# Performance work log

Measured on AMD Instinct MI355X. Metric: run time of the kernel, lower is better.

Reference implementation:

```python
import jax, jax.numpy as jnp
import numpy as np
import math

B, S, HID, H = 8, 512, 768, 12
D = HID // H  # 64
LABEL_VOCAB = 2 * 40 + 1  # 81
EPS = 1e-5


def layernorm(x, g, b):
    mu = jnp.mean(x, axis=-1, keepdims=True)
    var = jnp.var(x, axis=-1, keepdims=True)
    return (x - mu) * jax.lax.rsqrt(var + EPS) * g + b


def setup_inputs() -> dict:
    key = jax.random.key(0)
    ks = jax.random.split(key, 12)
    s = 0.02
    return {
        "hidden_states": jax.random.normal(ks[0], (B, S, HID), jnp.float32),
        "attention_mask": jnp.zeros((B, 1, 1, S), jnp.float32),
        "graph_arc": jax.random.randint(ks[1], (B, S, S), 0, LABEL_VOCAB, jnp.int32),
        "Wq": jax.random.normal(ks[2], (HID, HID), jnp.float32) * s,
        "bq": jnp.zeros((HID,), jnp.float32),
        "Wk": jax.random.normal(ks[3], (HID, HID), jnp.float32) * s,
        "bk": jnp.zeros((HID,), jnp.float32),
        "Wv": jax.random.normal(ks[4], (HID, HID), jnp.float32) * s,
        "bv": jnp.zeros((HID,), jnp.float32),
        "rel_k": jax.random.normal(ks[5], (LABEL_VOCAB, D), jnp.float32) * s,
        "rel_v": jax.random.normal(ks[6], (LABEL_VOCAB, D), jnp.float32) * s,
        "ln_k_g": jnp.ones((D,), jnp.float32),
        "ln_k_b": jnp.zeros((D,), jnp.float32),
        "ln_v_g": jnp.ones((D,), jnp.float32),
        "ln_v_b": jnp.zeros((D,), jnp.float32),
    }


def reference(hidden_states, attention_mask, graph_arc, Wq, bq, Wk, bk, Wv, bv,
              rel_k, rel_v, ln_k_g, ln_k_b, ln_v_g, ln_v_b):
    # projections -> [B, H, S, D]
    def split_heads(x):
        return x.reshape(B, S, H, D).transpose(0, 2, 1, 3)

    q = split_heads(hidden_states @ Wq + bq)
    k = split_heads(hidden_states @ Wk + bk)
    v = split_heads(hidden_states @ Wv + bv)

    # relation embeddings [B, S, S, D], layernormed over D
    dp_keys = layernorm(rel_k[graph_arc], ln_k_g, ln_k_b)
    dp_values = layernorm(rel_v[graph_arc], ln_v_g, ln_v_b)

    scores = jnp.einsum('bhqd,bhkd->bhqk', q, k) / math.sqrt(D)
    # relative_matmul_dp: per (b, q-position) GEMM of q[B,S,H,D] with dp_keys^T
    scores = scores + jnp.einsum('bqhd,bqkd->bhqk', q.transpose(0, 2, 1, 3), dp_keys)
    scores = scores + attention_mask

    probs = jax.nn.softmax(scores, axis=-1)  # dropout p=0 (eval)

    ctx = jnp.einsum('bhqk,bhkd->bqhd', probs, v)
    # relative_matmul_dpv
    ctx = ctx + jnp.einsum('bhqk,bqkd->bqhd', probs, dp_values)
    return ctx.reshape(B, S, HID)
```

## Files before the change

### kernel.cpp

```cpp
#include <hip/hip_runtime.h>
#include <hip/hip_bf16.h>

#define BB 8
#define SS 512
#define HIDV 768
#define HH 12
#define DD 64
#define LV 81

typedef __attribute__((ext_vector_type(8))) short short8v;
typedef __attribute__((ext_vector_type(4))) short short4v;
typedef __attribute__((ext_vector_type(4))) float f32x4;

#define MFMA16(a, b, c) __builtin_amdgcn_mfma_f32_16x16x32_bf16(a, b, c, 0, 0, 0)

__device__ __forceinline__ short f2bf(float f) {
    __hip_bfloat16 h = __float2bfloat16(f);
    return *reinterpret_cast<short*>(&h);
}
__device__ __forceinline__ float bf2f(short s) {
    __hip_bfloat16 h = *reinterpret_cast<__hip_bfloat16*>(&s);
    return __bfloat162float(h);
}
__device__ __forceinline__ void gload16(const void* g, void* l) {
    __builtin_amdgcn_global_load_lds((const __attribute__((address_space(1))) void*)g,
                                     (__attribute__((address_space(3))) void*)l, 16, 0, 0);
}

__global__ __launch_bounds__(256) void prep_ln_kernel(
    const float* __restrict__ rel_k, const float* __restrict__ rel_v,
    const float* __restrict__ gk, const float* __restrict__ bk,
    const float* __restrict__ gv, const float* __restrict__ bv,
    short* __restrict__ lnkb, short* __restrict__ lnvT) {
    __shared__ float ln_lds[2 * LV][DD];
    int t = threadIdx.x;
    if (t < 2 * LV) {
        bool isv = (t >= LV);
        int r = isv ? t - LV : t;
        const float* row = (isv ? rel_v : rel_k) + r * DD;
        const float* g = isv ? gv : gk;
        const float* be = isv ? bv : bk;
        float mu = 0.f;
        for (int d = 0; d < DD; ++d) mu += row[d];
        mu *= (1.f / DD);
        float var = 0.f;
        for (int d = 0; d < DD; ++d) { float x = row[d] - mu; var += x * x; }
        var *= (1.f / DD);
        float rs = rsqrtf(var + 1e-5f);
        for (int d = 0; d < DD; ++d) ln_lds[t][d] = (row[d] - mu) * rs * g[d] + be[d];
    }
    __syncthreads();
    for (int i = t; i < 96 * DD; i += 256) {
        int l = i >> 6, d = i & 63;
        lnkb[i] = (l < LV) ? f2bf(ln_lds[l][d]) : (short)0;
    }
    for (int i = t; i < DD * 96; i += 256) {
        int d = i / 96, ll = i - d * 96;
        lnvT[i] = (ll < LV) ? f2bf(ln_lds[LV + ll][d]) : (short)0;
    }
}

__global__ __launch_bounds__(256) void conv_hidden_kernel(const float* __restrict__ in,
                                                          short* __restrict__ out) {
    int i = (blockIdx.x * 256 + threadIdx.x) * 4;
    float4 v = *reinterpret_cast<const float4*>(&in[i]);
    short4v o; o[0] = f2bf(v.x); o[1] = f2bf(v.y); o[2] = f2bf(v.z); o[3] = f2bf(v.w);
    *reinterpret_cast<short4v*>(&out[i]) = o;
}

__global__ __launch_bounds__(256) void transw_kernel(
    const float* __restrict__ Wq, const float* __restrict__ Wk, const float* __restrict__ Wv,
    short* __restrict__ WqT, short* __restrict__ WkT, short* __restrict__ WvT) {
    const float* W; short* O;
    if (blockIdx.z == 0) { W = Wq; O = WqT; }
    else if (blockIdx.z == 1) { W = Wk; O = WkT; }
    else { W = Wv; O = WvT; }
    __shared__ float tile[32][33];
    int k0 = blockIdx.y * 32, n0 = blockIdx.x * 32;
    int t = threadIdx.x;
    int r = t >> 3, c4 = (t & 7) * 4;
    float4 v = *reinterpret_cast<const float4*>(&W[(size_t)(k0 + r) * HIDV + n0 + c4]);
    tile[r][c4 + 0] = v.x; tile[r][c4 + 1] = v.y; tile[r][c4 + 2] = v.z; tile[r][c4 + 3] = v.w;
    __syncthreads();
    short4v o;
    o[0] = f2bf(tile[c4 + 0][r]); o[1] = f2bf(tile[c4 + 1][r]);
    o[2] = f2bf(tile[c4 + 2][r]); o[3] = f2bf(tile[c4 + 3][r]);
    *reinterpret_cast<short4v*>(&O[(size_t)(n0 + r) * HIDV + k0 + c4]) = o;
}

__global__ __launch_bounds__(256) void qkv_gemm_kernel(
    const short* __restrict__ Abf,
    const short* __restrict__ WqT, const short* __restrict__ WkT, const short* __restrict__ WvT,
    const float* __restrict__ bq, const float* __restrict__ bk, const float* __restrict__ bv,
    short* __restrict__ qo, short* __restrict__ ko, short* __restrict__ vto) {
    const short* Bt; const float* bias;
    int z = blockIdx.z;
    if (z == 0) { Bt = WqT; bias = bq; }
    else if (z == 1) { Bt = WkT; bias = bk; }
    else { Bt = WvT; bias = bv; }

    __shared__ short smem[8192];
    short* As = smem;
    short* Bs = smem + 4096;

    const int tid = threadIdx.x;
    const int lane = tid & 63, w = tid >> 6;
    const int li = lane & 15, g = lane >> 4;
    const int wr = w >> 1, wc = w & 1;
    const int m0 = blockIdx.y * 64, n0 = blockIdx.x * 64;

    f32x4 acc[2][2];
    for (int ra = 0; ra < 2; ++ra)
        for (int cb = 0; cb < 2; ++cb)
            for (int r = 0; r < 4; ++r) acc[ra][cb][r] = 0.f;

#pragma unroll 1
    for (int k0 = 0; k0 < HIDV; k0 += 64) {
#pragma unroll
        for (int j = 0; j < 2; ++j) {
            int c = j * 256 + tid;
            int row = c >> 3, s = c & 7;
            int src = s ^ (row & 7);
// ... 38 lines not shown
                float bv_ = bias[n0 + n];
#pragma unroll
                for (int r = 0; r < 4; ++r) {
                    int m = m0 + 32 * wr + 16 * ra + 4 * g + r;
                    int s = m & 511;
                    dst[(((size_t)bidx * HH + h) * SS + s) * DD + n] =
                        f2bf((acc[ra][cb][r] + bv_) * sc);
                }
            }
    } else {
        short* Cs = smem;
#pragma unroll
        for (int ra = 0; ra < 2; ++ra)
#pragma unroll
            for (int cb = 0; cb < 2; ++cb) {
                int nl = 32 * wc + 16 * cb + li;
                float bv_ = bias[n0 + nl];
#pragma unroll
                for (int r = 0; r < 4; ++r) {
                    int ml = 32 * wr + 16 * ra + 4 * g + r;
                    Cs[nl * 72 + ml] = f2bf(acc[ra][cb][r] + bv_);
                }
            }
        __syncthreads();
        for (int c = tid; c < 512; c += 256) {
            int dl = c >> 3, s8 = (c & 7) * 8;
            short8v vv = *reinterpret_cast<const short8v*>(&Cs[dl * 72 + s8]);
            *reinterpret_cast<short8v*>(
                &vto[(((size_t)bidx * HH + h) * DD + dl) * SS + (m0 & 511) + s8]) = vv;
        }
    }
}

__global__ __launch_bounds__(256, 2) void attn_kernel(
    const short* __restrict__ qb, const short* __restrict__ kb, const short* __restrict__ vt,
    const int* __restrict__ arc, const float* __restrict__ mask,
    const short* __restrict__ lnkb, const short* __restrict__ lnvT,
    float* __restrict__ outp) {
    __shared__ short Ks[2][64][64];
    __shared__ short Vs[64][64];
    __shared__ float qlds[4][16][82];
    __shared__ float bucket[4][16][96];
    __shared__ short pl[4][16][72];

    const int tid = threadIdx.x;
    const int w = tid >> 6, lane = tid & 63;
    const int li = lane & 15, g = lane >> 4;
    const int bx = blockIdx.x;
    const int b = bx & 7;
    const int rest = bx >> 3;
    const int h = rest % HH, qt = rest / HH;
    const int bh = b * HH + h;
    const int q0 = qt * 64 + w * 16;

    const short* kbp = kb + (size_t)bh * SS * DD;
    const short* vbp = vt + (size_t)bh * DD * SS;
    const int* arcb = arc + ((size_t)b * SS + qt * 64) * SS;
    const float* maskb = mask + b * SS;

#pragma unroll
    for (int j = 0; j < 2; ++j) {
        int c = tid + 256 * j, row = c >> 3, s8 = (c & 7) ^ (row & 7);
        gload16(kbp + (size_t)row * DD + s8 * 8, &Ks[0][0][0] + c * 8);
    }
    for (int i = lane; i < 16 * 96; i += 64) (&bucket[w][0][0])[i] = 0.f;

    short8v qf[2];
    {
        const short* qrow = qb + ((size_t)bh * SS + q0 + li) * DD + 8 * g;
        qf[0] = *reinterpret_cast<const short8v*>(qrow);
        qf[1] = *reinterpret_cast<const short8v*>(qrow + 32);
    }

    {
        f32x4 qr[6];
        __builtin_amdgcn_s_setprio(1);
#pragma unroll
        for (int ct = 0; ct < 6; ++ct) {
            f32x4 a = {0.f, 0.f, 0.f, 0.f};
            short8v b0 = *reinterpret_cast<const short8v*>(&lnkb[(16 * ct + li) * DD + 8 * g]);
            short8v b1 = *reinterpret_cast<const short8v*>(&lnkb[(16 * ct + li) * DD + 32 + 8 * g]);
            a = MFMA16(qf[0], b0, a);
            a = MFMA16(qf[1], b1, a);
            qr[ct] = a;
        }
        __builtin_amdgcn_s_setprio(0);
#pragma unroll
        for (int ct = 0; ct < 6; ++ct)
#pragma unroll
            for (int r = 0; r < 4; ++r)
                if (16 * ct + li < 82) qlds[w][4 * g + r][16 * ct + li] = qr[ct][r];
    }

    f32x4 oacc[4];
    for (int t = 0; t < 4; ++t) for (int r = 0; r < 4; ++r) oacc[t][r] = 0.f;
    float lsum[4] = {0.f, 0.f, 0.f, 0.f};

#pragma unroll
    for (int kt = 0; kt < 8; ++kt) {
        const int cur = kt & 1, nxt = cur ^ 1;
        const int kb0 = kt * 64;

#pragma unroll
        for (int j = 0; j < 2; ++j) {
            int c = tid + 256 * j, row = c >> 3, s8 = (c & 7) ^ (row & 7);
            gload16(vbp + (size_t)row * SS + kb0 + s8 * 8, &Vs[0][0] + c * 8);
        }
        if (kt < 7) {
#pragma unroll
            for (int j = 0; j < 2; ++j) {
                int c = tid + 256 * j, row = c >> 3, s8 = (c & 7) ^ (row & 7);
                gload16(kbp + (size_t)(kb0 + 64 + row) * DD + s8 * 8, &Ks[nxt][0][0] + c * 8);
            }
            asm volatile("s_waitcnt vmcnt(4)" ::: "memory");
        } else {
            asm volatile("s_waitcnt vmcnt(2)" ::: "memory");
        }
        __builtin_amdgcn_sched_barrier(0);
        __builtin_amdgcn_s_barrier();
        __builtin_amdgcn_sched_barrier(0);

        int arcv[16];
        float mv[4];
#pragma unroll
        for (int t = 0; t < 4; ++t) {
            mv[t] = maskb[kb0 + 16 * t + li];
#pragma unroll
            for (int r = 0; r < 4; ++r)
                arcv[4 * t + r] = arcb[(size_t)(w * 16 + 4 * g + r) * SS + kb0 + 16 * t + li];
        }

        f32x4 sacc[4];
        __builtin_amdgcn_s_setprio(1);
#pragma unroll
        for (int t = 0; t < 4; ++t) {
            int row = 16 * t + li;
            short8v kf0 = *reinterpret_cast<const short8v*>(&Ks[cur][row][((g) ^ (li & 7)) * 8]);
            short8v kf1 = *reinterpret_cast<const short8v*>(&Ks[cur][row][((4 + g) ^ (li & 7)) * 8]);
            f32x4 a = {0.f, 0.f, 0.f, 0.f};
            a = MFMA16(qf[0], kf0, a);
            a = MFMA16(qf[1], kf1, a);
            sacc[t] = a;
        }
        __builtin_amdgcn_s_setprio(0);

#pragma unroll
        for (int t = 0; t < 4; ++t) {
#pragma unroll
            for (int r = 0; r < 4; ++r) {
                const int a_ = arcv[4 * t + r];
                const int row = 4 * g + r;
                float s = sacc[t][r] + qlds[w][row][a_] + mv[t];
                float p = __expf(s);
                lsum[r] += p;
                atomicAdd(&bucket[w][row][a_], p);
                pl[w][row][16 * t + li] = f2bf(p);
            }
        }

        if (kt < 7) asm volatile("s_waitcnt vmcnt(2)" ::: "memory");
        else        asm volatile("s_waitcnt vmcnt(0)" ::: "memory");
        __builtin_amdgcn_sched_barrier(0);
        __builtin_amdgcn_s_barrier();
        __builtin_amdgcn_sched_barrier(0);

        short8v pf0 = *reinterpret_cast<const short8v*>(&pl[w][li][8 * g]);
        short8v pf1 = *reinterpret_cast<const short8v*>(&pl[w][li][8 * g + 32]);
        __builtin_amdgcn_s_setprio(1);
#pragma unroll
        for (int t2 = 0; t2 < 4; ++t2) {
            int row = 16 * t2 + li;
            short8v vf0 = *reinterpret_cast<const short8v*>(&Vs[row][((g) ^ (li & 7)) * 8]);
            short8v vf1 = *reinterpret_cast<const short8v*>(&Vs[row][((4 + g) ^ (li & 7)) * 8]);
            oacc[t2] = MFMA16(pf0, vf0, oacc[t2]);
            oacc[t2] = MFMA16(pf1, vf1, oacc[t2]);
        }
        __builtin_amdgcn_s_setprio(0);

        if (kt < 7) {
            __builtin_amdgcn_s_barrier();
            __builtin_amdgcn_sched_barrier(0);
        }
    }

#pragma unroll
    for (int off = 1; off < 16; off <<= 1)
#pragma unroll
        for (int r = 0; r < 4; ++r) lsum[r] += __shfl_xor(lsum[r], off);

    f32x4 racc[4];
    for (int t = 0; t < 4; ++t) for (int r = 0; r < 4; ++r) racc[t][r] = 0.f;
#pragma unroll
    for (int c = 0; c < 3; ++c) {
        f32x4 b0 = *reinterpret_cast<const f32x4*>(&bucket[w][li][8 * g + 32 * c]);
        f32x4 b1 = *reinterpret_cast<const f32x4*>(&bucket[w][li][8 * g + 32 * c + 4]);
        short8v bfr;
        bfr[0] = f2bf(b0[0]); bfr[1] = f2bf(b0[1]); bfr[2] = f2bf(b0[2]); bfr[3] = f2bf(b0[3]);
        bfr[4] = f2bf(b1[0]); bfr[5] = f2bf(b1[1]); bfr[6] = f2bf(b1[2]); bfr[7] = f2bf(b1[3]);
#pragma unroll
        for (int t2 = 0; t2 < 4; ++t2) {
            short8v lf = *reinterpret_cast<const short8v*>(
                &lnvT[(16 * t2 + li) * 96 + 8 * g + 32 * c]);
            racc[t2] = MFMA16(bfr, lf, racc[t2]);
        }
    }

    float inv[4];
#pragma unroll
    for (int r = 0; r < 4; ++r) inv[r] = 1.f / lsum[r];

#pragma unroll
    for (int t2 = 0; t2 < 4; ++t2)
#pragma unroll
        for (int r = 0; r < 4; ++r) {
            int row = q0 + 4 * g + r;
            outp[((size_t)b * SS + row) * HIDV + h * DD + 16 * t2 + li] =
                (oacc[t2][r] + racc[t2][r]) * inv[r];
        }
}

extern "C" void kernel_launch(void* const* d_in, const int* in_sizes, int n_in,
                              void* d_out, int out_size, void* d_ws, size_t ws_size,
                              hipStream_t stream) {
    const float* hidden = (const float*)d_in[0];
    const float* mask   = (const float*)d_in[1];
    const int*   arc    = (const int*)d_in[2];
    const float* Wq = (const float*)d_in[3];
    const float* bq = (const float*)d_in[4];
    const float* Wk = (const float*)d_in[5];
    const float* bk = (const float*)d_in[6];
    const float* Wv = (const float*)d_in[7];
    const float* bv = (const float*)d_in[8];
    const float* rel_k = (const float*)d_in[9];
    const float* rel_v = (const float*)d_in[10];
    const float* lng_k = (const float*)d_in[11];
    const float* lnb_k = (const float*)d_in[12];
    const float* lng_v = (const float*)d_in[13];
    const float* lnb_v = (const float*)d_in[14];
    float* out = (float*)d_out;

    char* p = (char*)d_ws;
    auto carve = [&](size_t bytes) { char* r = p; p += (bytes + 255) & ~(size_t)255; return r; };
    short* lnkb = (short*)carve((size_t)96 * DD * 2);
    short* lnvT = (short*)carve((size_t)DD * 96 * 2);
    short* hbf  = (short*)carve((size_t)BB * SS * HIDV * 2);
    short* WqT  = (short*)carve((size_t)HIDV * HIDV * 2);
    short* WkT  = (short*)carve((size_t)HIDV * HIDV * 2);
    short* WvT  = (short*)carve((size_t)HIDV * HIDV * 2);
    const size_t per = (size_t)BB * HH * SS * DD;
    short* qbuf = (short*)carve(per * 2);
    short* kbuf = (short*)carve(per * 2);
    short* vtb  = (short*)carve(per * 2);

    prep_ln_kernel<<<1, 256, 0, stream>>>(rel_k, rel_v, lng_k, lnb_k, lng_v, lnb_v, lnkb, lnvT);
    conv_hidden_kernel<<<(BB * SS * HIDV) / 1024, 256, 0, stream>>>(hidden, hbf);
    transw_kernel<<<dim3(24, 24, 3), 256, 0, stream>>>(Wq, Wk, Wv, WqT, WkT, WvT);
    qkv_gemm_kernel<<<dim3(HIDV / 64, (BB * SS) / 64, 3), 256, 0, stream>>>(
        hbf, WqT, WkT, WvT, bq, bk, bv, qbuf, kbuf, vtb);
    attn_kernel<<<dim3(BB * HH * 8), 256, 0, stream>>>(
        qbuf, kbuf, vtb, arc, mask, lnkb, lnvT, out);
}
```

Measured before the change: 201.6 us.

## Pre-pack arc indices to transposed uint8 and stream them into LDS per tile

Adds a kernel that converts the int32 graph_arc tensor into a transposed uint8 layout, so the attention kernel reads a quarter of the bytes. The attention kernel now loads each 64x64 arc tile into LDS asynchronously alongside the K/V loads, and caches the mask as bf16 in LDS. It also drops the s_setprio hints, moves the loop barrier to the top of each iteration, and trims the qlds/bucket padding to 81/84. The cost is an extra prepass kernel that reads the full arc tensor once. The bf16 mask is lossy for general mask values, and the padding changes alter LDS bank patterns.

```diff
diff --git a/kernel.cpp b/kernel.cpp
--- a/kernel.cpp
+++ b/kernel.cpp
@@ -88,6 +88,28 @@
     *reinterpret_cast<short4v*>(&O[(size_t)(n0 + r) * HIDV + k0 + c4]) = o;
 }
 
+__global__ __launch_bounds__(256) void arct_kernel(const int* __restrict__ arc,
+                                                   unsigned char* __restrict__ arcT) {
+    __shared__ unsigned char t8[64][68];
+    const int tid = threadIdx.x;
+    const int bz = blockIdx.z;
+    const int q0 = blockIdx.y * 64, k0 = blockIdx.x * 64;
+    for (int i = tid; i < 64 * 16; i += 256) {
+        int r = i >> 4, c4 = (i & 15) * 4;
+        int4 v = *reinterpret_cast<const int4*>(&arc[((size_t)(bz * SS) + q0 + r) * SS + k0 + c4]);
+        t8[c4 + 0][r] = (unsigned char)v.x;
+        t8[c4 + 1][r] = (unsigned char)v.y;
+        t8[c4 + 2][r] = (unsigned char)v.z;
+        t8[c4 + 3][r] = (unsigned char)v.w;
+    }
+    __syncthreads();
+    for (int i = tid; i < 64 * 16; i += 256) {
+        int c = i >> 4, r4 = (i & 15) * 4;
+        unsigned int vv = *reinterpret_cast<const unsigned int*>(&t8[c][r4]);
+        *reinterpret_cast<unsigned int*>(&arcT[((size_t)(bz * SS) + k0 + c) * SS + q0 + r4]) = vv;
+    }
+}
+
 __global__ __launch_bounds__(256) void qkv_gemm_kernel(
     const short* __restrict__ Abf,
     const short* __restrict__ WqT, const short* __restrict__ WkT, const short* __restrict__ WvT,
@@ -194,13 +216,15 @@
 
 __global__ __launch_bounds__(256, 2) void attn_kernel(
     const short* __restrict__ qb, const short* __restrict__ kb, const short* __restrict__ vt,
-    const int* __restrict__ arc, const float* __restrict__ mask,
+    const unsigned char* __restrict__ arcT, const float* __restrict__ mask,
     const short* __restrict__ lnkb, const short* __restrict__ lnvT,
     float* __restrict__ outp) {
     __shared__ short Ks[2][64][64];
     __shared__ short Vs[64][64];
-    __shared__ float qlds[4][16][82];
-    __shared__ float bucket[4][16][96];
+    __shared__ unsigned char As[4096];
+    __shared__ short maskL[512];
+    __shared__ float qlds[4][16][81];
+    __shared__ float bucket[4][16][84];
     __shared__ short pl[4][16][72];
 
     const int tid = threadIdx.x;
@@ -211,19 +235,20 @@
     const int rest = bx >> 3;
     const int h = rest % HH, qt = rest / HH;
     const int bh = b * HH + h;
-    const int q0 = qt * 64 + w * 16;
+    const int q0b = qt * 64;
+    const int q0 = q0b + w * 16;
 
     const short* kbp = kb + (size_t)bh * SS * DD;
     const short* vbp = vt + (size_t)bh * DD * SS;
-    const int* arcb = arc + ((size_t)b * SS + qt * 64) * SS;
-    const float* maskb = mask + b * SS;
+    const unsigned char* abp = arcT + (size_t)b * SS * SS;
 
 #pragma unroll
     for (int j = 0; j < 2; ++j) {
         int c = tid + 256 * j, row = c >> 3, s8 = (c & 7) ^ (row & 7);
         gload16(kbp + (size_t)row * DD + s8 * 8, &Ks[0][0][0] + c * 8);
     }
-    for (int i = lane; i < 16 * 96; i += 64) (&bucket[w][0][0])[i] = 0.f;
+    for (int i = tid; i < SS; i += 256) maskL[i] = f2bf(mask[b * SS + i]);
+    for (int i = lane; i < 16 * 84; i += 64) (&bucket[w][0][0])[i] = 0.f;
 
     short8v qf[2];
     {
@@ -234,7 +259,6 @@
 
     {
         f32x4 qr[6];
-        __builtin_amdgcn_s_setprio(1);
 #pragma unroll
         for (int ct = 0; ct < 6; ++ct) {
             f32x4 a = {0.f, 0.f, 0.f, 0.f};
@@ -244,13 +268,13 @@
             a = MFMA16(qf[1], b1, a);
             qr[ct] = a;
         }
-        __builtin_amdgcn_s_setprio(0);
 #pragma unroll
         for (int ct = 0; ct < 6; ++ct)
 #pragma unroll
             for (int r = 0; r < 4; ++r)
-                if (16 * ct + li < 82) qlds[w][4 * g + r][16 * ct + li] = qr[ct][r];
-    }
+                if (16 * ct + li < 81) qlds[w][4 * g + r][16 * ct + li] = qr[ct][r];
+    }
+    asm volatile("s_waitcnt lgkmcnt(0)" ::: "memory");
 
     f32x4 oacc[4];
     for (int t = 0; t < 4; ++t) for (int r = 0; r < 4; ++r) oacc[t][r] = 0.f;
@@ -261,17 +285,29 @@
         const int cur = kt & 1, nxt = cur ^ 1;
         const int kb0 = kt * 64;
 
+        __builtin_amdgcn_sched_barrier(0);
+        __builtin_amdgcn_s_barrier();
+        __builtin_amdgcn_sched_barrier(0);
+
+        {
+            int col = tid >> 2, seg = tid & 3;
+            int sc_ = seg ^ (col & 3);
+            gload16(abp + (size_t)(kb0 + col) * SS + q0b + sc_ * 16, As + tid * 16);
+        }
+        __builtin_amdgcn_sched_barrier(0);
 #pragma unroll
         for (int j = 0; j < 2; ++j) {
             int c = tid + 256 * j, row = c >> 3, s8 = (c & 7) ^ (row & 7);
             gload16(vbp + (size_t)row * SS + kb0 + s8 * 8, &Vs[0][0] + c * 8);
         }
+        __builtin_amdgcn_sched_barrier(0);
         if (kt < 7) {
 #pragma unroll
             for (int j = 0; j < 2; ++j) {
                 int c = tid + 256 * j, row = c >> 3, s8 = (c & 7) ^ (row & 7);
                 gload16(kbp + (size_t)(kb0 + 64 + row) * DD + s8 * 8, &Ks[nxt][0][0] + c * 8);
             }
+            __builtin_amdgcn_sched_barrier(0);
             asm volatile("s_waitcnt vmcnt(4)" ::: "memory");
         } else {
             asm volatile("s_waitcnt vmcnt(2)" ::: "memory");
@@ -280,18 +316,7 @@
         __builtin_amdgcn_s_barrier();
         __builtin_amdgcn_sched_barrier(0);
 
-        int arcv[16];
-        float mv[4];
-#pragma unroll
-        for (int t = 0; t < 4; ++t) {
-            mv[t] = maskb[kb0 + 16 * t + li];
-#pragma unroll
-            for (int r = 0; r < 4; ++r)
-                arcv[4 * t + r] = arcb[(size_t)(w * 16 + 4 * g + r) * SS + kb0 + 16 * t + li];
-        }
-
         f32x4 sacc[4];
-        __builtin_amdgcn_s_setprio(1);
 #pragma unroll
         for (int t = 0; t < 4; ++t) {
             int row = 16 * t + li;
@@ -302,19 +327,22 @@
             a = MFMA16(qf[1], kf1, a);
             sacc[t] = a;
         }
-        __builtin_amdgcn_s_setprio(0);
 
 #pragma unroll
         for (int t = 0; t < 4; ++t) {
+            const int col = 16 * t + li;
+            const float mval = bf2f(maskL[kb0 + col]);
+            unsigned int a4 = *reinterpret_cast<const unsigned int*>(
+                &As[col * 64 + (((w ^ (col & 3)) << 4) | (g << 2))]);
 #pragma unroll
             for (int r = 0; r < 4; ++r) {
-                const int a_ = arcv[4 * t + r];
+                const int a_ = (a4 >> (8 * r)) & 255;
                 const int row = 4 * g + r;
-                float s = sacc[t][r] + qlds[w][row][a_] + mv[t];
+                float s = sacc[t][r] + qlds[w][row][a_] + mval;
                 float p = __expf(s);
                 lsum[r] += p;
                 atomicAdd(&bucket[w][row][a_], p);
-                pl[w][row][16 * t + li] = f2bf(p);
+                pl[w][row][col] = f2bf(p);
             }
         }
 
@@ -326,7 +354,6 @@
 
         short8v pf0 = *reinterpret_cast<const short8v*>(&pl[w][li][8 * g]);
         short8v pf1 = *reinterpret_cast<const short8v*>(&pl[w][li][8 * g + 32]);
-        __builtin_amdgcn_s_setprio(1);
 #pragma unroll
         for (int t2 = 0; t2 < 4; ++t2) {
             int row = 16 * t2 + li;
@@ -335,12 +362,6 @@
             oacc[t2] = MFMA16(pf0, vf0, oacc[t2]);
             oacc[t2] = MFMA16(pf1, vf1, oacc[t2]);
         }
-        __builtin_amdgcn_s_setprio(0);
-
-        if (kt < 7) {
-            __builtin_amdgcn_s_barrier();
-            __builtin_amdgcn_sched_barrier(0);
-        }
     }
 
 #pragma unroll
@@ -352,8 +373,18 @@
     for (int t = 0; t < 4; ++t) for (int r = 0; r < 4; ++r) racc[t][r] = 0.f;
 #pragma unroll
     for (int c = 0; c < 3; ++c) {
-        f32x4 b0 = *reinterpret_cast<const f32x4*>(&bucket[w][li][8 * g + 32 * c]);
-        f32x4 b1 = *reinterpret_cast<const f32x4*>(&bucket[w][li][8 * g + 32 * c + 4]);
+        f32x4 b0, b1;
+        if (c < 2) {
+            b0 = *reinterpret_cast<const f32x4*>(&bucket[w][li][8 * g + 32 * c]);
+            b1 = *reinterpret_cast<const f32x4*>(&bucket[w][li][8 * g + 32 * c + 4]);
+        } else {
+#pragma unroll
+            for (int e = 0; e < 4; ++e) {
+                int c0 = 64 + 8 * g + e, c1 = c0 + 4;
+                b0[e] = (c0 < 81) ? bucket[w][li][c0] : 0.f;
+                b1[e] = (c1 < 81) ? bucket[w][li][c1] : 0.f;
+            }
+        }
         short8v bfr;
         bfr[0] = f2bf(b0[0]); bfr[1] = f2bf(b0[1]); bfr[2] = f2bf(b0[2]); bfr[3] = f2bf(b0[3]);
         bfr[4] = f2bf(b1[0]); bfr[5] = f2bf(b1[1]); bfr[6] = f2bf(b1[2]); bfr[7] = f2bf(b1[3]);
@@ -411,12 +442,14 @@
     short* qbuf = (short*)carve(per * 2);
     short* kbuf = (short*)carve(per * 2);
     short* vtb  = (short*)carve(per * 2);
+    unsigned char* arcT8 = (unsigned char*)carve((size_t)BB * SS * SS);
 
     prep_ln_kernel<<<1, 256, 0, stream>>>(rel_k, rel_v, lng_k, lnb_k, lng_v, lnb_v, lnkb, lnvT);
     conv_hidden_kernel<<<(BB * SS * HIDV) / 1024, 256, 0, stream>>>(hidden, hbf);
     transw_kernel<<<dim3(24, 24, 3), 256, 0, stream>>>(Wq, Wk, Wv, WqT, WkT, WvT);
+    arct_kernel<<<dim3(8, 8, BB), 256, 0, stream>>>(arc, arcT8);
     qkv_gemm_kernel<<<dim3(HIDV / 64, (BB * SS) / 64, 3), 256, 0, stream>>>(
         hbf, WqT, WkT, WvT, bq, bk, bv, qbuf, kbuf, vtb);
     attn_kernel<<<dim3(BB * HH * 8), 256, 0, stream>>>(
-        qbuf, kbuf, vtb, arc, mask, lnkb, lnvT, out);
-}
+        qbuf, kbuf, vtb, arcT8, mask, lnkb, lnvT, out);
+}
```

Result: slower. 205.7 us (+2.0%).

## Pack arc labels to bytes and drop LDS staging in attention kernel

Applied to the files above, without the earlier changes.

Adds a pre-pass kernel that packs the int32 arc labels into bytes, transposed so each lane of the attention kernel reads four labels in one coalesced 32-bit load. The arc matrix is otherwise re-read by all 12 heads, so this shrinks that traffic. The attention kernel also drops LDS staging and barriers for K and V and loads fragments straight from global memory. It computes S^T so probabilities stay in registers as the A operand for the PV MFMA instead of round-tripping through LDS, and occupancy rises to 3 blocks per SM. The risks are uncoalesced direct global loads for K and V, and an extra kernel launch plus its memory pass.

```diff
diff --git a/kernel.cpp b/kernel.cpp
--- a/kernel.cpp
+++ b/kernel.cpp
@@ -88,6 +88,25 @@
     *reinterpret_cast<short4v*>(&O[(size_t)(n0 + r) * HIDV + k0 + c4]) = o;
 }
 
+__global__ __launch_bounds__(256) void arcpack_kernel(const int* __restrict__ arc,
+                                                      unsigned int* __restrict__ arcP) {
+    __shared__ unsigned int tbuf[64][129];
+    const int tid = threadIdx.x;
+    const int b = blockIdx.y;
+    const int q0 = blockIdx.x * 64;
+    for (int i = tid; i < 64 * 128; i += 256) {
+        int r = i >> 7, c4 = i & 127;
+        int4 v = *reinterpret_cast<const int4*>(&arc[((size_t)(b * SS) + q0 + r) * SS + 4 * c4]);
+        tbuf[r][c4] = (unsigned)(v.x & 255) | ((unsigned)(v.y & 255) << 8) |
+                      ((unsigned)(v.z & 255) << 16) | ((unsigned)(v.w & 255) << 24);
+    }
+    __syncthreads();
+    for (int i = tid; i < 128 * 64; i += 256) {
+        int k4 = i >> 6, r = i & 63;
+        arcP[((size_t)b * 128 + k4) * SS + q0 + r] = tbuf[r][k4];
+    }
+}
+
 __global__ __launch_bounds__(256) void qkv_gemm_kernel(
     const short* __restrict__ Abf,
     const short* __restrict__ WqT, const short* __restrict__ WkT, const short* __restrict__ WvT,
@@ -192,16 +211,13 @@
     }
 }
 
-__global__ __launch_bounds__(256, 2) void attn_kernel(
+__global__ __launch_bounds__(256, 3) void attn_kernel(
     const short* __restrict__ qb, const short* __restrict__ kb, const short* __restrict__ vt,
-    const int* __restrict__ arc, const float* __restrict__ mask,
+    const unsigned int* __restrict__ arcP, const float* __restrict__ maskp,
     const short* __restrict__ lnkb, const short* __restrict__ lnvT,
     float* __restrict__ outp) {
-    __shared__ short Ks[2][64][64];
-    __shared__ short Vs[64][64];
-    __shared__ float qlds[4][16][82];
+    __shared__ float qlds[4][16][84];
     __shared__ float bucket[4][16][96];
-    __shared__ short pl[4][16][72];
 
     const int tid = threadIdx.x;
     const int w = tid >> 6, lane = tid & 63;
@@ -215,14 +231,7 @@
 
     const short* kbp = kb + (size_t)bh * SS * DD;
     const short* vbp = vt + (size_t)bh * DD * SS;
-    const int* arcb = arc + ((size_t)b * SS + qt * 64) * SS;
-    const float* maskb = mask + b * SS;
-
-#pragma unroll
-    for (int j = 0; j < 2; ++j) {
-        int c = tid + 256 * j, row = c >> 3, s8 = (c & 7) ^ (row & 7);
-        gload16(kbp + (size_t)row * DD + s8 * 8, &Ks[0][0][0] + c * 8);
-    }
+
     for (int i = lane; i < 16 * 96; i += 64) (&bucket[w][0][0])[i] = 0.f;
 
     short8v qf[2];
@@ -234,7 +243,6 @@
 
     {
         f32x4 qr[6];
-        __builtin_amdgcn_s_setprio(1);
 #pragma unroll
         for (int ct = 0; ct < 6; ++ct) {
             f32x4 a = {0.f, 0.f, 0.f, 0.f};
@@ -244,109 +252,82 @@
             a = MFMA16(qf[1], b1, a);
             qr[ct] = a;
         }
-        __builtin_amdgcn_s_setprio(0);
 #pragma unroll
         for (int ct = 0; ct < 6; ++ct)
 #pragma unroll
             for (int r = 0; r < 4; ++r)
-                if (16 * ct + li < 82) qlds[w][4 * g + r][16 * ct + li] = qr[ct][r];
+                if (16 * ct + li < 84) qlds[w][4 * g + r][16 * ct + li] = qr[ct][r];
     }
 
     f32x4 oacc[4];
     for (int t = 0; t < 4; ++t) for (int r = 0; r < 4; ++r) oacc[t][r] = 0.f;
-    float lsum[4] = {0.f, 0.f, 0.f, 0.f};
-
-#pragma unroll
+    float lsum = 0.f;
+
+#pragma unroll 2
     for (int kt = 0; kt < 8; ++kt) {
-        const int cur = kt & 1, nxt = cur ^ 1;
         const int kb0 = kt * 64;
 
-#pragma unroll
-        for (int j = 0; j < 2; ++j) {
-            int c = tid + 256 * j, row = c >> 3, s8 = (c & 7) ^ (row & 7);
-            gload16(vbp + (size_t)row * SS + kb0 + s8 * 8, &Vs[0][0] + c * 8);
-        }
-        if (kt < 7) {
-#pragma unroll
-            for (int j = 0; j < 2; ++j) {
-                int c = tid + 256 * j, row = c >> 3, s8 = (c & 7) ^ (row & 7);
-                gload16(kbp + (size_t)(kb0 + 64 + row) * DD + s8 * 8, &Ks[nxt][0][0] + c * 8);
-            }
-            asm volatile("s_waitcnt vmcnt(4)" ::: "memory");
-        } else {
-            asm volatile("s_waitcnt vmcnt(2)" ::: "memory");
-        }
-        __builtin_amdgcn_sched_barrier(0);
-        __builtin_amdgcn_s_barrier();
-        __builtin_amdgcn_sched_barrier(0);
-
-        int arcv[16];
-        float mv[4];
+        unsigned int a4[4];
+#pragma unroll
+        for (int t = 0; t < 4; ++t)
+            a4[t] = arcP[((size_t)b * 128 + kt * 16 + 4 * t + g) * SS + q0 + li];
+
+        float4 mv[4];
+#pragma unroll
+        for (int t = 0; t < 4; ++t)
+            mv[t] = *reinterpret_cast<const float4*>(&maskp[(size_t)b * SS + kb0 + 16 * t + 4 * g]);
+
+        f32x4 sacc[4];
 #pragma unroll
         for (int t = 0; t < 4; ++t) {
-            mv[t] = maskb[kb0 + 16 * t + li];
-#pragma unroll
-            for (int r = 0; r < 4; ++r)
-                arcv[4 * t + r] = arcb[(size_t)(w * 16 + 4 * g + r) * SS + kb0 + 16 * t + li];
-        }
-
-        f32x4 sacc[4];
-        __builtin_amdgcn_s_setprio(1);
+            const short* kr = kbp + (size_t)(kb0 + 16 * t + li) * DD + 8 * g;
+            short8v k0 = *reinterpret_cast<const short8v*>(kr);
+            short8v k1 = *reinterpret_cast<const short8v*>(kr + 32);
+            f32x4 a = {0.f, 0.f, 0.f, 0.f};
+            a = MFMA16(k0, qf[0], a);
+            a = MFMA16(k1, qf[1], a);
+            sacc[t] = a;
+        }
+
+        short8v pfrag[2];
 #pragma unroll
         for (int t = 0; t < 4; ++t) {
-            int row = 16 * t + li;
-            short8v kf0 = *reinterpret_cast<const short8v*>(&Ks[cur][row][((g) ^ (li & 7)) * 8]);
-            short8v kf1 = *reinterpret_cast<const short8v*>(&Ks[cur][row][((4 + g) ^ (li & 7)) * 8]);
-            f32x4 a = {0.f, 0.f, 0.f, 0.f};
-            a = MFMA16(qf[0], kf0, a);
-            a = MFMA16(qf[1], kf1, a);
-            sacc[t] = a;
-        }
-        __builtin_amdgcn_s_setprio(0);
-
-#pragma unroll
-        for (int t = 0; t < 4; ++t) {
+            float pv[4];
 #pragma unroll
             for (int r = 0; r < 4; ++r) {
-                const int a_ = arcv[4 * t + r];
-                const int row = 4 * g + r;
-                float s = sacc[t][r] + qlds[w][row][a_] + mv[t];
+                const int a_ = (a4[t] >> (8 * r)) & 255;
+                float s = sacc[t][r] + qlds[w][li][a_] +
+                          reinterpret_cast<const float*>(&mv[t])[r];
                 float p = __expf(s);
-                lsum[r] += p;
-                atomicAdd(&bucket[w][row][a_], p);
-                pl[w][row][16 * t + li] = f2bf(p);
-            }
-        }
-
-        if (kt < 7) asm volatile("s_waitcnt vmcnt(2)" ::: "memory");
-        else        asm volatile("s_waitcnt vmcnt(0)" ::: "memory");
-        __builtin_amdgcn_sched_barrier(0);
-        __builtin_amdgcn_s_barrier();
-        __builtin_amdgcn_sched_barrier(0);
-
-        short8v pf0 = *reinterpret_cast<const short8v*>(&pl[w][li][8 * g]);
-        short8v pf1 = *reinterpret_cast<const short8v*>(&pl[w][li][8 * g + 32]);
-        __builtin_amdgcn_s_setprio(1);
-#pragma unroll
-        for (int t2 = 0; t2 < 4; ++t2) {
-            int row = 16 * t2 + li;
-            short8v vf0 = *reinterpret_cast<const short8v*>(&Vs[row][((g) ^ (li & 7)) * 8]);
-            short8v vf1 = *reinterpret_cast<const short8v*>(&Vs[row][((4 + g) ^ (li & 7)) * 8]);
-            oacc[t2] = MFMA16(pf0, vf0, oacc[t2]);
-            oacc[t2] = MFMA16(pf1, vf1, oacc[t2]);
-        }
-        __builtin_amdgcn_s_setprio(0);
-
-        if (kt < 7) {
-            __builtin_amdgcn_s_barrier();
-            __builtin_amdgcn_sched_barrier(0);
-        }
-    }
-
-#pragma unroll
-    for (int off = 1; off < 16; off <<= 1)
-#pragma unroll
-        for (int r = 0; r < 4; ++r) lsum[r] += __shfl_xor(lsum[r], off);
+                lsum += p;
+                atomicAdd(&bucket[w][li][a_], p);
+                pv[r] = p;
+            }
+#pragma unroll
+            for (int r = 0; r < 4; ++r) pfrag[t >> 1][4 * (t & 1) + r] = f2bf(pv[r]);
+        }
+
+#pragma unroll
+        for (int dt = 0; dt < 2; ++dt) {
+#pragma unroll
+            for (int t2 = 0; t2 < 4; ++t2) {
+                const short* vr = vbp + (size_t)(16 * t2 + li) * SS + kb0 + 32 * dt + 4 * g;
+                short4v v0 = *reinterpret_cast<const short4v*>(vr);
+                short4v v1 = *reinterpret_cast<const short4v*>(vr + 16);
+                short8v vf;
+                vf[0] = v0[0]; vf[1] = v0[1]; vf[2] = v0[2]; vf[3] = v0[3];
+                vf[4] = v1[0]; vf[5] = v1[1]; vf[6] = v1[2]; vf[7] = v1[3];
+                oacc[t2] = MFMA16(pfrag[dt], vf, oacc[t2]);
+            }
+        }
+    }
+
+    lsum += __shfl_xor(lsum, 16);
+    lsum += __shfl_xor(lsum, 32);
+    float inv = 1.f / lsum;
+    float invr[4];
+#pragma unroll
+    for (int r = 0; r < 4; ++r) invr[r] = __shfl(inv, 4 * g + r);
 
     f32x4 racc[4];
     for (int t = 0; t < 4; ++t) for (int r = 0; r < 4; ++r) racc[t][r] = 0.f;
@@ -365,17 +346,13 @@
         }
     }
 
-    float inv[4];
-#pragma unroll
-    for (int r = 0; r < 4; ++r) inv[r] = 1.f / lsum[r];
-
 #pragma unroll
     for (int t2 = 0; t2 < 4; ++t2)
 #pragma unroll
         for (int r = 0; r < 4; ++r) {
             int row = q0 + 4 * g + r;
             outp[((size_t)b * SS + row) * HIDV + h * DD + 16 * t2 + li] =
-                (oacc[t2][r] + racc[t2][r]) * inv[r];
+                (oacc[t2][r] + racc[t2][r]) * invr[r];
         }
 }
 
@@ -411,12 +388,14 @@
     short* qbuf = (short*)carve(per * 2);
     short* kbuf = (short*)carve(per * 2);
     short* vtb  = (short*)carve(per * 2);
+    unsigned int* arcP = (unsigned int*)carve((size_t)BB * 128 * SS * 4);
 
     prep_ln_kernel<<<1, 256, 0, stream>>>(rel_k, rel_v, lng_k, lnb_k, lng_v, lnb_v, lnkb, lnvT);
     conv_hidden_kernel<<<(BB * SS * HIDV) / 1024, 256, 0, stream>>>(hidden, hbf);
     transw_kernel<<<dim3(24, 24, 3), 256, 0, stream>>>(Wq, Wk, Wv, WqT, WkT, WvT);
+    arcpack_kernel<<<dim3(8, BB), 256, 0, stream>>>(arc, arcP);
     qkv_gemm_kernel<<<dim3(HIDV / 64, (BB * SS) / 64, 3), 256, 0, stream>>>(
         hbf, WqT, WkT, WvT, bq, bk, bv, qbuf, kbuf, vtb);
     attn_kernel<<<dim3(BB * HH * 8), 256, 0, stream>>>(
-        qbuf, kbuf, vtb, arc, mask, lnkb, lnvT, out);
-}
+        qbuf, kbuf, vtb, arcP, mask, lnkb, lnvT, out);
+}
```

Result: no change. 199.0 us (-1.3%).

## Split fused attention into scores and PV kernels with packed arc and bucket columns

Applied to the files above, without the earlier changes.

The single fused attention kernel becomes two kernels. The first computes exp scores and the per-label probability buckets and writes a bf16 P matrix of width 640 to workspace: 512 key columns plus 96 bucket columns and padding. The second runs one GEMM of that P against V concatenated with the transposed relation values, then normalises by the stored row sums. A new pre-pass packs graph_arc to bytes transposed in groups of four query rows, so each lane gets four labels in one 32-bit load. Work runs in two chunks of 48 batch-heads so the P buffer can reuse the workspace tail. This trades the extra global round trip for P against a more regular GEMM structure with 2x2 warp tiles.

```diff
diff --git a/kernel.cpp b/kernel.cpp
--- a/kernel.cpp
+++ b/kernel.cpp
@@ -31,7 +31,7 @@
     const float* __restrict__ rel_k, const float* __restrict__ rel_v,
     const float* __restrict__ gk, const float* __restrict__ bk,
     const float* __restrict__ gv, const float* __restrict__ bv,
-    short* __restrict__ lnkb, short* __restrict__ lnvT) {
+    short* __restrict__ lnkb, short* __restrict__ lnvT128) {
     __shared__ float ln_lds[2 * LV][DD];
     int t = threadIdx.x;
     if (t < 2 * LV) {
@@ -54,9 +54,9 @@
         int l = i >> 6, d = i & 63;
         lnkb[i] = (l < LV) ? f2bf(ln_lds[l][d]) : (short)0;
     }
-    for (int i = t; i < DD * 96; i += 256) {
-        int d = i / 96, ll = i - d * 96;
-        lnvT[i] = (ll < LV) ? f2bf(ln_lds[LV + ll][d]) : (short)0;
+    for (int i = t; i < DD * 128; i += 256) {
+        int d = i >> 7, l = i & 127;
+        lnvT128[i] = (l < LV) ? f2bf(ln_lds[LV + l][d]) : (short)0;
     }
 }
 
@@ -88,6 +88,32 @@
     *reinterpret_cast<short4v*>(&O[(size_t)(n0 + r) * HIDV + k0 + c4]) = o;
 }
 
+__global__ __launch_bounds__(256) void arcq_kernel(const int* __restrict__ arc,
+                                                   unsigned int* __restrict__ arcQ) {
+    __shared__ unsigned char t8[64][68];
+    const int tid = threadIdx.x;
+    const int b = blockIdx.z;
+    const int q0 = blockIdx.y * 64, k0 = blockIdx.x * 64;
+    for (int i = tid; i < 64 * 16; i += 256) {
+        int q = i >> 4, kc = (i & 15) * 4;
+        int4 v = *reinterpret_cast<const int4*>(&arc[((size_t)(b * SS) + q0 + q) * SS + k0 + kc]);
+        t8[kc + 0][q] = (unsigned char)v.x;
+        t8[kc + 1][q] = (unsigned char)v.y;
+        t8[kc + 2][q] = (unsigned char)v.z;
+        t8[kc + 3][q] = (unsigned char)v.w;
+    }
+    __syncthreads();
+    {
+        int q4 = tid >> 4, kb = (tid & 15) * 4;
+        uint4 o;
+        o.x = *reinterpret_cast<const unsigned int*>(&t8[kb + 0][4 * q4]);
+        o.y = *reinterpret_cast<const unsigned int*>(&t8[kb + 1][4 * q4]);
+        o.z = *reinterpret_cast<const unsigned int*>(&t8[kb + 2][4 * q4]);
+        o.w = *reinterpret_cast<const unsigned int*>(&t8[kb + 3][4 * q4]);
+        *reinterpret_cast<uint4*>(&arcQ[((size_t)b * 128 + (q0 >> 2) + q4) * SS + k0 + kb]) = o;
+    }
+}
+
 __global__ __launch_bounds__(256) void qkv_gemm_kernel(
     const short* __restrict__ Abf,
     const short* __restrict__ WqT, const short* __restrict__ WkT, const short* __restrict__ WvT,
@@ -192,190 +218,279 @@
     }
 }
 
-__global__ __launch_bounds__(256, 2) void attn_kernel(
-    const short* __restrict__ qb, const short* __restrict__ kb, const short* __restrict__ vt,
-    const int* __restrict__ arc, const float* __restrict__ mask,
-    const short* __restrict__ lnkb, const short* __restrict__ lnvT,
-    float* __restrict__ outp) {
+__global__ __launch_bounds__(256, 2) void scores_kernel(
+    const short* __restrict__ qb, const short* __restrict__ kb,
+    const unsigned int* __restrict__ arcQ, const float* __restrict__ maskp,
+    const short* __restrict__ lnkb,
+    short* __restrict__ Pbuf, float* __restrict__ rowsum, int bh0) {
     __shared__ short Ks[2][64][64];
-    __shared__ short Vs[64][64];
-    __shared__ float qlds[4][16][82];
-    __shared__ float bucket[4][16][96];
-    __shared__ short pl[4][16][72];
+    __shared__ float qlds[64][84];
+    __shared__ float bucket[64][96];
+    __shared__ float rowsumL[64];
 
     const int tid = threadIdx.x;
     const int w = tid >> 6, lane = tid & 63;
     const int li = lane & 15, g = lane >> 4;
+    const int wr = w >> 1, wc = w & 1;
     const int bx = blockIdx.x;
-    const int b = bx & 7;
-    const int rest = bx >> 3;
+    const int bL = bx & 3, rest = bx >> 2;
     const int h = rest % HH, qt = rest / HH;
+    const int b = bh0 / HH + bL;
     const int bh = b * HH + h;
-    const int q0 = qt * 64 + w * 16;
+    const int bhL = bh - bh0;
+    const int q0 = qt * 64;
 
     const short* kbp = kb + (size_t)bh * SS * DD;
-    const short* vbp = vt + (size_t)bh * DD * SS;
-    const int* arcb = arc + ((size_t)b * SS + qt * 64) * SS;
-    const float* maskb = mask + b * SS;
+    short* pbp = Pbuf + (size_t)bhL * SS * 640;
 
 #pragma unroll
     for (int j = 0; j < 2; ++j) {
         int c = tid + 256 * j, row = c >> 3, s8 = (c & 7) ^ (row & 7);
         gload16(kbp + (size_t)row * DD + s8 * 8, &Ks[0][0][0] + c * 8);
     }
-    for (int i = lane; i < 16 * 96; i += 64) (&bucket[w][0][0])[i] = 0.f;
-
-    short8v qf[2];
-    {
-        const short* qrow = qb + ((size_t)bh * SS + q0 + li) * DD + 8 * g;
-        qf[0] = *reinterpret_cast<const short8v*>(qrow);
-        qf[1] = *reinterpret_cast<const short8v*>(qrow + 32);
-    }
-
-    {
-        f32x4 qr[6];
-        __builtin_amdgcn_s_setprio(1);
-#pragma unroll
-        for (int ct = 0; ct < 6; ++ct) {
-            f32x4 a = {0.f, 0.f, 0.f, 0.f};
-            short8v b0 = *reinterpret_cast<const short8v*>(&lnkb[(16 * ct + li) * DD + 8 * g]);
-            short8v b1 = *reinterpret_cast<const short8v*>(&lnkb[(16 * ct + li) * DD + 32 + 8 * g]);
-            a = MFMA16(qf[0], b0, a);
-            a = MFMA16(qf[1], b1, a);
-            qr[ct] = a;
-        }
-        __builtin_amdgcn_s_setprio(0);
-#pragma unroll
-        for (int ct = 0; ct < 6; ++ct)
-#pragma unroll
-            for (int r = 0; r < 4; ++r)
-                if (16 * ct + li < 82) qlds[w][4 * g + r][16 * ct + li] = qr[ct][r];
-    }
-
-    f32x4 oacc[4];
-    for (int t = 0; t < 4; ++t) for (int r = 0; r < 4; ++r) oacc[t][r] = 0.f;
-    float lsum[4] = {0.f, 0.f, 0.f, 0.f};
+    for (int i = tid; i < 64 * 96; i += 256) (&bucket[0][0])[i] = 0.f;
+    if (tid < 64) rowsumL[tid] = 0.f;
+
+    short8v af[2][2];
+#pragma unroll
+    for (int ra = 0; ra < 2; ++ra) {
+        const short* base = qb + ((size_t)bh * SS + q0 + 32 * wr + 16 * ra + li) * DD + 8 * g;
+        af[ra][0] = *reinterpret_cast<const short8v*>(base);
+        af[ra][1] = *reinterpret_cast<const short8v*>(base + 32);
+    }
+
+    float mvv[8][2];
+    unsigned int av[8][2][2];
+    const int q4base = (q0 + 32 * wr) >> 2;
+#pragma unroll
+    for (int kt = 0; kt < 8; ++kt) {
+#pragma unroll
+        for (int cb = 0; cb < 2; ++cb) {
+            mvv[kt][cb] = maskp[(size_t)b * SS + kt * 64 + 32 * wc + 16 * cb + li];
+#pragma unroll
+            for (int ra = 0; ra < 2; ++ra)
+                av[kt][ra][cb] = arcQ[((size_t)b * 128 + q4base + 4 * ra + g) * SS +
+                                      kt * 64 + 32 * wc + 16 * cb + li];
+        }
+    }
+
+    if (wc == 0) {
+#pragma unroll
+        for (int ra = 0; ra < 2; ++ra)
+#pragma unroll
+            for (int ct = 0; ct < 6; ++ct) {
+                f32x4 a = {0.f, 0.f, 0.f, 0.f};
+                short8v b0 = *reinterpret_cast<const short8v*>(&lnkb[(16 * ct + li) * DD + 8 * g]);
+                short8v b1 = *reinterpret_cast<const short8v*>(&lnkb[(16 * ct + li) * DD + 32 + 8 * g]);
+                a = MFMA16(af[ra][0], b0, a);
+                a = MFMA16(af[ra][1], b1, a);
+                int col = 16 * ct + li;
+                if (col < 84)
+#pragma unroll
+                    for (int r = 0; r < 4; ++r)
+                        qlds[32 * wr + 16 * ra + 4 * g + r][col] = a[r];
+            }
+    }
+    asm volatile("s_waitcnt lgkmcnt(0)" ::: "memory");
+    __builtin_amdgcn_sched_barrier(0);
+
+    float rsum[2][4];
+#pragma unroll
+    for (int ra = 0; ra < 2; ++ra)
+#pragma unroll
+        for (int r = 0; r < 4; ++r) rsum[ra][r] = 0.f;
 
 #pragma unroll
     for (int kt = 0; kt < 8; ++kt) {
         const int cur = kt & 1, nxt = cur ^ 1;
         const int kb0 = kt * 64;
 
-#pragma unroll
-        for (int j = 0; j < 2; ++j) {
-            int c = tid + 256 * j, row = c >> 3, s8 = (c & 7) ^ (row & 7);
-            gload16(vbp + (size_t)row * SS + kb0 + s8 * 8, &Vs[0][0] + c * 8);
-        }
         if (kt < 7) {
 #pragma unroll
             for (int j = 0; j < 2; ++j) {
                 int c = tid + 256 * j, row = c >> 3, s8 = (c & 7) ^ (row & 7);
                 gload16(kbp + (size_t)(kb0 + 64 + row) * DD + s8 * 8, &Ks[nxt][0][0] + c * 8);
             }
-            asm volatile("s_waitcnt vmcnt(4)" ::: "memory");
+            __builtin_amdgcn_sched_barrier(0);
+            asm volatile("s_waitcnt vmcnt(2)" ::: "memory");
         } else {
-            asm volatile("s_waitcnt vmcnt(2)" ::: "memory");
+            asm volatile("s_waitcnt vmcnt(0)" ::: "memory");
         }
         __builtin_amdgcn_sched_barrier(0);
         __builtin_amdgcn_s_barrier();
         __builtin_amdgcn_sched_barrier(0);
 
-        int arcv[16];
-        float mv[4];
-#pragma unroll
-        for (int t = 0; t < 4; ++t) {
-            mv[t] = maskb[kb0 + 16 * t + li];
+        f32x4 acc[2][2];
+#pragma unroll
+        for (int ra = 0; ra < 2; ++ra)
+#pragma unroll
+            for (int cb = 0; cb < 2; ++cb)
+                for (int r = 0; r < 4; ++r) acc[ra][cb][r] = 0.f;
+#pragma unroll
+        for (int c = 0; c < 2; ++c) {
+            short8v bf[2];
+#pragma unroll
+            for (int cb = 0; cb < 2; ++cb) {
+                int rowb = 32 * wc + 16 * cb + li;
+                int chunk = (4 * c + g) ^ (rowb & 7);
+                bf[cb] = *reinterpret_cast<const short8v*>(&Ks[cur][rowb][chunk * 8]);
+            }
+#pragma unroll
+            for (int ra = 0; ra < 2; ++ra)
+#pragma unroll
+                for (int cb = 0; cb < 2; ++cb)
+                    acc[ra][cb] = MFMA16(af[ra][c], bf[cb], acc[ra][cb]);
+        }
+
+#pragma unroll
+        for (int ra = 0; ra < 2; ++ra)
+#pragma unroll
+            for (int cb = 0; cb < 2; ++cb) {
+                const unsigned int a4 = av[kt][ra][cb];
+                const float m = mvv[kt][cb];
+                const int colk = kb0 + 32 * wc + 16 * cb + li;
+                const int rowb = 32 * wr + 16 * ra + 4 * g;
+#pragma unroll
+                for (int r = 0; r < 4; ++r) {
+                    const int a_ = (a4 >> (8 * r)) & 255;
+                    float s = acc[ra][cb][r] + qlds[rowb + r][a_] + m;
+                    float p = __expf(s);
+                    rsum[ra][r] += p;
+                    atomicAdd(&bucket[rowb + r][a_], p);
+                    pbp[(size_t)(q0 + rowb + r) * 640 + colk] = f2bf(p);
+                }
+            }
+
+        __builtin_amdgcn_s_barrier();
+        __builtin_amdgcn_sched_barrier(0);
+    }
+
+#pragma unroll
+    for (int m = 1; m < 16; m <<= 1)
+#pragma unroll
+        for (int ra = 0; ra < 2; ++ra)
+#pragma unroll
+            for (int r = 0; r < 4; ++r) rsum[ra][r] += __shfl_xor(rsum[ra][r], m);
+    if (li == 0) {
+#pragma unroll
+        for (int ra = 0; ra < 2; ++ra)
 #pragma unroll
             for (int r = 0; r < 4; ++r)
-                arcv[4 * t + r] = arcb[(size_t)(w * 16 + 4 * g + r) * SS + kb0 + 16 * t + li];
-        }
-
-        f32x4 sacc[4];
-        __builtin_amdgcn_s_setprio(1);
-#pragma unroll
-        for (int t = 0; t < 4; ++t) {
-            int row = 16 * t + li;
-            short8v kf0 = *reinterpret_cast<const short8v*>(&Ks[cur][row][((g) ^ (li & 7)) * 8]);
-            short8v kf1 = *reinterpret_cast<const short8v*>(&Ks[cur][row][((4 + g) ^ (li & 7)) * 8]);
-            f32x4 a = {0.f, 0.f, 0.f, 0.f};
-            a = MFMA16(qf[0], kf0, a);
-            a = MFMA16(qf[1], kf1, a);
-            sacc[t] = a;
-        }
-        __builtin_amdgcn_s_setprio(0);
-
-#pragma unroll
-        for (int t = 0; t < 4; ++t) {
-#pragma unroll
-            for (int r = 0; r < 4; ++r) {
-                const int a_ = arcv[4 * t + r];
-                const int row = 4 * g + r;
-                float s = sacc[t][r] + qlds[w][row][a_] + mv[t];
-                float p = __expf(s);
-                lsum[r] += p;
-                atomicAdd(&bucket[w][row][a_], p);
-                pl[w][row][16 * t + li] = f2bf(p);
-            }
-        }
-
-        if (kt < 7) asm volatile("s_waitcnt vmcnt(2)" ::: "memory");
-        else        asm volatile("s_waitcnt vmcnt(0)" ::: "memory");
+                atomicAdd(&rowsumL[32 * wr + 16 * ra + 4 * g + r], rsum[ra][r]);
+    }
+    __syncthreads();
+
+    for (int i = tid; i < 64 * 96; i += 256) {
+        int row = i / 96, l = i - row * 96;
+        pbp[(size_t)(q0 + row) * 640 + 512 + l] = f2bf(bucket[row][l]);
+    }
+    if (tid < 64) rowsum[(size_t)bh * SS + q0 + tid] = rowsumL[tid];
+}
+
+__global__ __launch_bounds__(256, 2) void pv_kernel(
+    const short* __restrict__ Pbuf, const short* __restrict__ vt,
+    const short* __restrict__ lnvT128, const float* __restrict__ rowsum,
+    float* __restrict__ outp, int bh0) {
+    __shared__ short As[2][64][64];
+    __shared__ short Bs[2][64][64];
+
+    const int tid = threadIdx.x;
+    const int w = tid >> 6, lane = tid & 63;
+    const int li = lane & 15, g = lane >> 4;
+    const int wr = w >> 1, wc = w & 1;
+    const int bx = blockIdx.x;
+    const int bL = bx & 3, rest = bx >> 2;
+    const int h = rest % HH, qt = rest / HH;
+    const int b = bh0 / HH + bL;
+    const int bh = b * HH + h;
+    const int bhL = bh - bh0;
+    const int q0 = qt * 64;
+
+    const short* pbp = Pbuf + (size_t)bhL * SS * 640;
+    const short* vbp = vt + (size_t)bh * DD * SS;
+
+#pragma unroll
+    for (int j = 0; j < 2; ++j) {
+        int c = tid + 256 * j, row = c >> 3, s8 = (c & 7) ^ (row & 7);
+        gload16(pbp + (size_t)(q0 + row) * 640 + s8 * 8, &As[0][0][0] + c * 8);
+        gload16(vbp + (size_t)row * SS + s8 * 8, &Bs[0][0][0] + c * 8);
+    }
+
+    f32x4 acc[2][2];
+#pragma unroll
+    for (int ra = 0; ra < 2; ++ra)
+#pragma unroll
+        for (int cb = 0; cb < 2; ++cb)
+            for (int r = 0; r < 4; ++r) acc[ra][cb][r] = 0.f;
+
+#pragma unroll
+    for (int it = 0; it < 10; ++it) {
+        const int cur = it & 1, nxt = cur ^ 1;
+
+        if (it < 9) {
+            const int kk = (it + 1) * 64;
+#pragma unroll
+            for (int j = 0; j < 2; ++j) {
+                int c = tid + 256 * j, row = c >> 3, s8 = (c & 7) ^ (row & 7);
+                gload16(pbp + (size_t)(q0 + row) * 640 + kk + s8 * 8, &As[nxt][0][0] + c * 8);
+                if (kk < 512)
+                    gload16(vbp + (size_t)row * SS + kk + s8 * 8, &Bs[nxt][0][0] + c * 8);
+                else
+                    gload16(lnvT128 + (size_t)row * 128 + (kk - 512) + s8 * 8, &Bs[nxt][0][0] + c * 8);
+            }
+            __builtin_amdgcn_sched_barrier(0);
+            asm volatile("s_waitcnt vmcnt(4)" ::: "memory");
+        } else {
+            asm volatile("s_waitcnt vmcnt(0)" ::: "memory");
+        }
         __builtin_amdgcn_sched_barrier(0);
         __builtin_amdgcn_s_barrier();
         __builtin_amdgcn_sched_barrier(0);
 
-        short8v pf0 = *reinterpret_cast<const short8v*>(&pl[w][li][8 * g]);
-        short8v pf1 = *reinterpret_cast<const short8v*>(&pl[w][li][8 * g + 32]);
-        __builtin_amdgcn_s_setprio(1);
-#pragma unroll
-        for (int t2 = 0; t2 < 4; ++t2) {
-            int row = 16 * t2 + li;
-            short8v vf0 = *reinterpret_cast<const short8v*>(&Vs[row][((g) ^ (li & 7)) * 8]);
-            short8v vf1 = *reinterpret_cast<const short8v*>(&Vs[row][((4 + g) ^ (li & 7)) * 8]);
-            oacc[t2] = MFMA16(pf0, vf0, oacc[t2]);
-            oacc[t2] = MFMA16(pf1, vf1, oacc[t2]);
-        }
-        __builtin_amdgcn_s_setprio(0);
-
-        if (kt < 7) {
-            __builtin_amdgcn_s_barrier();
-            __builtin_amdgcn_sched_barrier(0);
-        }
-    }
-
-#pragma unroll
-    for (int off = 1; off < 16; off <<= 1)
-#pragma unroll
-        for (int r = 0; r < 4; ++r) lsum[r] += __shfl_xor(lsum[r], off);
-
-    f32x4 racc[4];
-    for (int t = 0; t < 4; ++t) for (int r = 0; r < 4; ++r) racc[t][r] = 0.f;
-#pragma unroll
-    for (int c = 0; c < 3; ++c) {
-        f32x4 b0 = *reinterpret_cast<const f32x4*>(&bucket[w][li][8 * g + 32 * c]);
-        f32x4 b1 = *reinterpret_cast<const f32x4*>(&bucket[w][li][8 * g + 32 * c + 4]);
-        short8v bfr;
-        bfr[0] = f2bf(b0[0]); bfr[1] = f2bf(b0[1]); bfr[2] = f2bf(b0[2]); bfr[3] = f2bf(b0[3]);
-        bfr[4] = f2bf(b1[0]); bfr[5] = f2bf(b1[1]); bfr[6] = f2bf(b1[2]); bfr[7] = f2bf(b1[3]);
-#pragma unroll
-        for (int t2 = 0; t2 < 4; ++t2) {
-            short8v lf = *reinterpret_cast<const short8v*>(
-                &lnvT[(16 * t2 + li) * 96 + 8 * g + 32 * c]);
-            racc[t2] = MFMA16(bfr, lf, racc[t2]);
-        }
-    }
-
-    float inv[4];
-#pragma unroll
-    for (int r = 0; r < 4; ++r) inv[r] = 1.f / lsum[r];
-
-#pragma unroll
-    for (int t2 = 0; t2 < 4; ++t2)
-#pragma unroll
-        for (int r = 0; r < 4; ++r) {
-            int row = q0 + 4 * g + r;
-            outp[((size_t)b * SS + row) * HIDV + h * DD + 16 * t2 + li] =
-                (oacc[t2][r] + racc[t2][r]) * inv[r];
+#pragma unroll
+        for (int c = 0; c < 2; ++c) {
+            short8v af[2], bf[2];
+#pragma unroll
+            for (int ra = 0; ra < 2; ++ra) {
+                int row = 32 * wr + 16 * ra + li;
+                int chunk = (4 * c + g) ^ (row & 7);
+                af[ra] = *reinterpret_cast<const short8v*>(&As[cur][row][chunk * 8]);
+            }
+#pragma unroll
+            for (int cb = 0; cb < 2; ++cb) {
+                int rowb = 32 * wc + 16 * cb + li;
+                int chunk = (4 * c + g) ^ (rowb & 7);
+                bf[cb] = *reinterpret_cast<const short8v*>(&Bs[cur][rowb][chunk * 8]);
+            }
+#pragma unroll
+            for (int ra = 0; ra < 2; ++ra)
+#pragma unroll
+                for (int cb = 0; cb < 2; ++cb)
+                    acc[ra][cb] = MFMA16(af[ra], bf[cb], acc[ra][cb]);
+        }
+
+        __builtin_amdgcn_s_barrier();
+        __builtin_amdgcn_sched_barrier(0);
+    }
+
+    float invv[2][4];
+#pragma unroll
+    for (int ra = 0; ra < 2; ++ra)
+#pragma unroll
+        for (int r = 0; r < 4; ++r)
+            invv[ra][r] = 1.f / rowsum[(size_t)bh * SS + q0 + 32 * wr + 16 * ra + 4 * g + r];
+
+#pragma unroll
+    for (int ra = 0; ra < 2; ++ra)
+#pragma unroll
+        for (int cb = 0; cb < 2; ++cb) {
+            int col = 32 * wc + 16 * cb + li;
+#pragma unroll
+            for (int r = 0; r < 4; ++r) {
+                int row = q0 + 32 * wr + 16 * ra + 4 * g + r;
+                outp[((size_t)b * SS + row) * HIDV + h * DD + col] =
+                    acc[ra][cb][r] * invv[ra][r];
+            }
         }
 }
 
@@ -401,22 +516,31 @@
 
     char* p = (char*)d_ws;
     auto carve = [&](size_t bytes) { char* r = p; p += (bytes + 255) & ~(size_t)255; return r; };
-    short* lnkb = (short*)carve((size_t)96 * DD * 2);
-    short* lnvT = (short*)carve((size_t)DD * 96 * 2);
+    short* lnkb    = (short*)carve((size_t)96 * DD * 2);
+    short* lnvT128 = (short*)carve((size_t)DD * 128 * 2);
+    const size_t per = (size_t)BB * HH * SS * DD;
+    short* qbuf = (short*)carve(per * 2);
+    short* kbuf = (short*)carve(per * 2);
+    short* vtb  = (short*)carve(per * 2);
+    unsigned int* arcQ = (unsigned int*)carve((size_t)BB * 128 * SS * 4);
+    float* rowsum = (float*)carve((size_t)BB * HH * SS * 4);
+    char* tail = p;
     short* hbf  = (short*)carve((size_t)BB * SS * HIDV * 2);
     short* WqT  = (short*)carve((size_t)HIDV * HIDV * 2);
     short* WkT  = (short*)carve((size_t)HIDV * HIDV * 2);
     short* WvT  = (short*)carve((size_t)HIDV * HIDV * 2);
-    const size_t per = (size_t)BB * HH * SS * DD;
-    short* qbuf = (short*)carve(per * 2);
-    short* kbuf = (short*)carve(per * 2);
-    short* vtb  = (short*)carve(per * 2);
-
-    prep_ln_kernel<<<1, 256, 0, stream>>>(rel_k, rel_v, lng_k, lnb_k, lng_v, lnb_v, lnkb, lnvT);
+    short* Pbuf = (short*)tail;
+
+    prep_ln_kernel<<<1, 256, 0, stream>>>(rel_k, rel_v, lng_k, lnb_k, lng_v, lnb_v, lnkb, lnvT128);
     conv_hidden_kernel<<<(BB * SS * HIDV) / 1024, 256, 0, stream>>>(hidden, hbf);
     transw_kernel<<<dim3(24, 24, 3), 256, 0, stream>>>(Wq, Wk, Wv, WqT, WkT, WvT);
+    arcq_kernel<<<dim3(8, 8, BB), 256, 0, stream>>>(arc, arcQ);
     qkv_gemm_kernel<<<dim3(HIDV / 64, (BB * SS) / 64, 3), 256, 0, stream>>>(
         hbf, WqT, WkT, WvT, bq, bk, bv, qbuf, kbuf, vtb);
-    attn_kernel<<<dim3(BB * HH * 8), 256, 0, stream>>>(
-        qbuf, kbuf, vtb, arc, mask, lnkb, lnvT, out);
-}
+    for (int chunk = 0; chunk < 2; ++chunk) {
+        int bh0 = chunk * 48;
+        scores_kernel<<<dim3(384), 256, 0, stream>>>(qbuf, kbuf, arcQ, mask, lnkb,
+                                                     Pbuf, rowsum, bh0);
+        pv_kernel<<<dim3(384), 256, 0, stream>>>(Pbuf, vtb, lnvT128, rowsum, out, bh0);
+    }
+}
```

Measured after the change: 265.0 us. +31.4%, slower.
